# Kernel optimization log

Measured on AMD Instinct MI355X. Metric: run time of the kernel, lower is better.

## Reference

```python
import jax, jax.numpy as jnp
import numpy as np

H, N_EMB, D_EMB, D_UP = 1024, 8192, 512, 2048
B, T, BB, M, K_LABELS = 4, 4096, 512, 4096, 64


def _rms(x, w, eps=1e-6):
    xf = x.astype(jnp.float32)
    var = jnp.mean(xf * xf, axis=-1, keepdims=True)
    return (w * (xf * jax.lax.rsqrt(var + eps))).astype(x.dtype)


def setup_inputs() -> dict:
    key = jax.random.key(0)
    ks = jax.random.split(key, 8)
    bt = B * T
    inp = jax.random.normal(ks[0], (B, T, H), jnp.float32)
    w_k = jax.random.normal(ks[1], (N_EMB, H), jnp.float32) * 0.02
    w_v = jax.random.normal(ks[2], (N_EMB, D_EMB), jnp.float32) * 0.02
    w_up = jax.random.normal(ks[3], (D_UP, D_EMB), jnp.float32) * 0.02
    w_mix = jax.random.normal(ks[4], (H, D_UP + H), jnp.float32) * 0.02
    fw = jax.random.permutation(ks[5], bt)
    bw = jnp.argsort(fw)  # inverse permutation
    seq_sort = jax.random.randint(ks[6], (bt,), 0, K_LABELS)
    keep_cols = jnp.arange(M)  # keep first M of N_EMB rows
    emb_alloc = jnp.arange(N_EMB) % K_LABELS  # every label present among kept rows
    starts = jnp.zeros((bt,), jnp.int32)
    ends = jnp.full((bt,), M, jnp.int32)
    return {
        'input': inp, 'fw': fw, 'bw': bw, 'seq_sort': seq_sort,
        'keep_cols': keep_cols, 'emb_alloc': emb_alloc,
        'starts': starts, 'ends': ends, 'bb': BB,
        'w_k_weight': w_k, 'w_v_weight': w_v, 'w_up_weight': w_up,
        'w_mix_weight': w_mix,
        'norm_in_weight': jnp.ones((H,), jnp.float32),
        'norm_out_weight': jnp.ones((D_UP,), jnp.float32),
    }


def reference(input, fw, bw, seq_sort, keep_cols, emb_alloc, starts, ends, bb,
              w_k_weight, w_v_weight, w_up_weight, w_mix_weight,
              norm_in_weight, norm_out_weight):
    b, t, h = input.shape
    A = _rms(input, norm_in_weight)                      # [b,t,h]
    Bm = w_k_weight[keep_cols]                           # [m,h]
    Cm = w_v_weight[keep_cols]                           # [m,d_emb]
    la = emb_alloc[keep_cols]                            # [m]
    A = A.reshape(-1, h)[fw].reshape(-1, bb, h)          # [nb,bb,h]
    ss = seq_sort.reshape(-1, bb)                        # [nb,bb]
    st = starts.reshape(-1, bb).min(axis=-1)             # [nb]
    en = ends.reshape(-1, bb).max(axis=-1)               # [nb]
    # ragged per-block slice B[start:end] expressed as a kv range mask,
    # combined with the equality mask seq_sort[q] == emb_alloc[kv]
    scores = jnp.einsum('nqh,kh->nqk', A, Bm)            # [nb,bb,m]
    kv = jnp.arange(Bm.shape[0])
    mask = ((ss[:, :, None] == la[None, None, :])
            & (kv[None, None, :] >= st[:, None, None])
            & (kv[None, None, :] < en[:, None, None]))
    scores = jnp.where(mask, scores, -jnp.inf)
    p = jax.nn.softmax(scores, axis=-1)
    comb = jnp.einsum('nqk,kd->nqd', p, Cm)              # [nb,bb,d_emb]
    d_emb = Cm.shape[-1]
    comb = comb.reshape(-1, d_emb)[bw].reshape(b, t, d_emb)
    up = comb @ w_up_weight.T                            # [b,t,d_up]
    cat = jnp.concatenate([_rms(up, norm_out_weight), input], axis=-1)
    return cat @ w_mix_weight.T                          # [b,t,h]
```

## Files before the change

### kernel.cpp

```cpp
#include <hip/hip_runtime.h>
#include <hip/hip_bf16.h>
#include <cstdint>
#include <cstddef>

#define Hh 1024
#define D_EMB 512
#define D_UP 2048
#define BT 16384
#define BB_ 512
#define Mm 4096
#define MmP 4160
#define NB 32
#define KL 64
#define NXCD 8

typedef __attribute__((ext_vector_type(4))) float f4;
typedef __attribute__((ext_vector_type(4))) __bf16 bf4;
typedef __attribute__((ext_vector_type(8))) __bf16 bf8;
typedef __attribute__((ext_vector_type(4))) float f32x4;

__device__ __forceinline__ void gl_lds16(const void* g, void* l) {
  __builtin_amdgcn_global_load_lds((__attribute__((address_space(1))) void*)g,
                                   (__attribute__((address_space(3))) void*)l, 16, 0, 0);
}

__global__ __launch_bounds__(256) void conv_bf16_kernel(const float* __restrict__ src,
                                                        __bf16* __restrict__ dst, int n4) {
  int i = blockIdx.x * 256 + threadIdx.x;
  if (i >= n4) return;
  f4 v = ((const f4*)src)[i];
  bf4 o = {(__bf16)v[0], (__bf16)v[1], (__bf16)v[2], (__bf16)v[3]};
  ((bf4*)dst)[i] = o;
}

__global__ __launch_bounds__(256) void gather_bf16_kernel(const float* __restrict__ src,
                                                          const int* __restrict__ idx,
                                                          __bf16* __restrict__ dst, int cols4) {
  int row = blockIdx.x;
  const f4* s = (const f4*)src + (size_t)idx[row] * cols4;
  bf4* d = (bf4*)dst + (size_t)row * cols4;
  for (int i = threadIdx.x; i < cols4; i += 256) {
    f4 v = s[i];
    bf4 o = {(__bf16)v[0], (__bf16)v[1], (__bf16)v[2], (__bf16)v[3]};
    d[i] = o;
  }
}

__global__ __launch_bounds__(256) void la_kernel(const int* __restrict__ keep,
                                                 const int* __restrict__ emb,
                                                 int* __restrict__ la, int m) {
  int i = blockIdx.x * 256 + threadIdx.x;
  if (i < m) la[i] = emb[keep[i]];
}

__global__ __launch_bounds__(256) void range_kernel(const int* __restrict__ starts,
                                                    const int* __restrict__ ends,
                                                    int* __restrict__ stA, int* __restrict__ enA) {
  int n = blockIdx.x;
  int t = threadIdx.x, lane = t & 63, wv = t >> 6;
  int s1 = min(starts[n * BB_ + t], starts[n * BB_ + t + 256]);
  int e1 = max(ends[n * BB_ + t], ends[n * BB_ + t + 256]);
#pragma unroll
  for (int off = 32; off; off >>= 1) {
    s1 = min(s1, __shfl_xor(s1, off));
    e1 = max(e1, __shfl_xor(e1, off));
  }
  __shared__ int ssh[4], esh[4];
  if (lane == 0) { ssh[wv] = s1; esh[wv] = e1; }
  __syncthreads();
  if (t == 0) {
    int s = ssh[0], e = esh[0];
#pragma unroll
    for (int k = 1; k < 4; ++k) { s = min(s, ssh[k]); e = max(e, esh[k]); }
    stA[n] = s; enA[n] = e;
  }
}

__global__ __launch_bounds__(256) void hist_kernel(const int* __restrict__ la,
                                                   int* __restrict__ goff) {
  __shared__ int cnt[KL];
  int tid = threadIdx.x;
  if (tid < KL) cnt[tid] = 0;
  __syncthreads();
  for (int k = tid; k < Mm; k += 256) atomicAdd(&cnt[la[k]], 1);
  __syncthreads();
  if (tid == 0) {
    int a = 0;
    for (int s = 0; s < KL; ++s) { goff[s] = a; a += cnt[s]; }
    goff[KL] = a;
  }
}

__global__ __launch_bounds__(256) void place_kernel(const int* __restrict__ la,
                                                    const int* __restrict__ keep,
                                                    const int* __restrict__ goff,
                                                    int* __restrict__ gk,
                                                    int* __restrict__ ridx) {
  int s = blockIdx.x;
  int tid = threadIdx.x, lane = tid & 63, wv = tid >> 6;
  __shared__ int wc[4];
  __shared__ int run;
  if (tid == 0) run = goff[s];
  __syncthreads();
  for (int base = 0; base < Mm; base += 256) {
    int k = base + tid;
    bool f = (la[k] == s);
    unsigned long long msk = __ballot(f);
    int myidx = __popcll(msk & ((1ull << lane) - 1ull));
    if (lane == 0) wc[wv] = __popcll(msk);
    __syncthreads();
    int woff = 0, tot = 0;
#pragma unroll
    for (int w = 0; w < 4; ++w) {
      if (w < wv) woff += wc[w];
      tot += wc[w];
    }
    int rbase = run;
    if (f) {
      int p = rbase + woff + myidx;
      gk[p] = k;
      ridx[p] = keep[k];
    }
    __syncthreads();
    if (tid == 0) run = rbase + tot;
    __syncthreads();
  }
}

__global__ __launch_bounds__(256) void lohi_kernel(const int* __restrict__ gk,
                                                   const int* __restrict__ goff,
                                                   const int* __restrict__ stA,
                                                   const int* __restrict__ enA,
                                                   int* __restrict__ loA, int* __restrict__ hiA) {
  int i = blockIdx.x * 256 + threadIdx.x;
  if (i >= NB * KL) return;
  int n = i / KL, s = i % KL;
  int b = goff[s], e = goff[s + 1];
  int st = stA[n], en = enA[n];
  int lo = b, hi = e;
  while (lo < hi) { int mid = (lo + hi) >> 1; if (gk[mid] < st) lo = mid + 1; else hi = mid; }
  int L = lo;
  lo = b; hi = e;
  while (lo < hi) { int mid = (lo + hi) >> 1; if (gk[mid] < en) lo = mid + 1; else hi = mid; }
  loA[i] = L;
  hiA[i] = lo;
}

__global__ __launch_bounds__(256) void vt_kernel(const float* __restrict__ wv_,
                                                 const int* __restrict__ ridx,
                                                 __bf16* __restrict__ VT) {
  int pb = blockIdx.x * 64;
  int db = blockIdx.y * 64;
  __shared__ float T[64][65];
  int t = threadIdx.x;
  int dl = t & 63, g = t >> 6;
  for (int i = g * 16; i < g * 16 + 16; ++i) {
    int pos = pb + i;
    float val = 0.f;
    if (pos < Mm) {
      int r = ridx[pos];
      val = wv_[(size_t)r * D_EMB + db + dl];
    }
    T[dl][i] = val;
  }
  __syncthreads();
  int pl = t & 63;
  for (int j = g * 16; j < g * 16 + 16; ++j) {
    VT[(size_t)(db + j) * MmP + pb + pl] = (__bf16)T[j][pl];
  }
}

__global__ __launch_bounds__(256) void qsort_kernel(const int* __restrict__ seq_sort,
                                                    int* __restrict__ qidx,
                                                    int* __restrict__ qoffA,
                                                    int* __restrict__ qcntA) {
  int n = blockIdx.x, tid = threadIdx.x;
  __shared__ int cnt[KL], pos[KL], pref[KL];
  if (tid < KL) cnt[tid] = 0;
  __syncthreads();
  int s0 = seq_sort[n * BB_ + tid];
  int s1 = seq_sort[n * BB_ + tid + 256];
  atomicAdd(&cnt[s0], 1);
  atomicAdd(&cnt[s1], 1);
  __syncthreads();
  if (tid == 0) {
    int a = 0;
    for (int s = 0; s < KL; ++s) { pref[s] = a; a += cnt[s]; }
  }
  __syncthreads();
  if (tid < KL) {
    pos[tid] = pref[tid];
    qoffA[n * KL + tid] = pref[tid];
    qcntA[n * KL + tid] = cnt[tid];
  }
  __syncthreads();
  int p0 = atomicAdd(&pos[s0], 1);
  qidx[n * BB_ + p0] = n * BB_ + tid;
  int p1 = atomicAdd(&pos[s1], 1);
  qidx[n * BB_ + p1] = n * BB_ + tid + 256;
}

__global__ __launch_bounds__(256) void rms_in_kernel(const float* __restrict__ input,
                                                     const int* __restrict__ bw,
                                                     const float* __restrict__ wn,
                                                     __bf16* __restrict__ Aperm,
                                                     __bf16* __restrict__ inb) {
  int wv = threadIdx.x >> 6, lane = threadIdx.x & 63;
  int j = blockIdx.x * 4 + wv;
  const f4* src = (const f4*)(input + (size_t)j * Hh);
  f4 v[4];
  float ss = 0.f;
#pragma unroll
  for (int c = 0; c < 4; ++c) {
    v[c] = src[c * 64 + lane];
    ss += v[c][0] * v[c][0] + v[c][1] * v[c][1] + v[c][2] * v[c][2] + v[c][3] * v[c][3];
  }
#pragma unroll
  for (int off = 32; off; off >>= 1) ss += __shfl_xor(ss, off);
  float sc = rsqrtf(ss * (1.f / Hh) + 1e-6f);
  bf4* dstI = (bf4*)(inb + (size_t)j * Hh);
#pragma unroll
  for (int c = 0; c < 4; ++c) {
    bf4 o = {(__bf16)v[c][0], (__bf16)v[c][1], (__bf16)v[c][2], (__bf16)v[c][3]};
    dstI[c * 64 + lane] = o;
  }
  int dj = bw[j];
  const f4* w4 = (const f4*)wn;
  bf4* dstA = (bf4*)(Aperm + (size_t)dj * Hh);
#pragma unroll
  for (int c = 0; c < 4; ++c) {
    f4 w = w4[c * 64 + lane];
    bf4 o = {(__bf16)(v[c][0] * sc * w[0]), (__bf16)(v[c][1] * sc * w[1]),
             (__bf16)(v[c][2] * sc * w[2]), (__bf16)(v[c][3] * sc * w[3])};
    dstA[c * 64 + lane] = o;
  }
}

__global__ __launch_bounds__(256, 2) void attn4_kernel(const __bf16* __restrict__ Aperm,
                                                       const __bf16* __restrict__ Ks,
                                                       const __bf16* __restrict__ VT,
                                                       const int* __restrict__ qidx,
                                                       const int* __restrict__ qoffA,
                                                       const int* __restrict__ qcntA,
                                                       const int* __restrict__ loA,
                                                       const int* __restrict__ hiA,
                                                       const int* __restrict__ fw,
                                                       __bf16* __restrict__ comb) {
  __shared__ __align__(16) __bf16 owb[4][16][528];
  int wv = threadIdx.x >> 6, lane = threadIdx.x & 63;
  int g = blockIdx.x * 4 + wv;
  int qcnt = qcntA[g];
  int lo = loA[g], hi = hiA[g];
  if (qcnt == 0 || lo >= hi) return;
  int n = g >> 6;
  int qbase = n * BB_ + qoffA[g];
  int c = lane & 15, rg = lane >> 4;
  int sl_a = c + ((rg & 1) << 5);
  int sl_b = sl_a + 16;
  bool hiKt = (rg & 2) != 0;
  const __bf16* vbase = VT + (size_t)c * MmP + rg * 8;

  for (int qt = 0; qt < qcnt; qt += 16) {
    int ql = qt + c;
    int j = qidx[qbase + (ql < qcnt ? ql : qcnt - 1)];
    const __bf16* qrow = Aperm + (size_t)j * Hh + rg * 8;

    float m = -1e30f, lsum = 0.f;
    f32x4 acc[32];
    f32x4 zero = {0.f, 0.f, 0.f, 0.f};
#pragma unroll
    for (int ff = 0; ff < 32; ++ff) acc[ff] = zero;

    for (int p0 = lo; p0 < hi; p0 += 64) {
      const __bf16* kb = Ks + (size_t)(p0 + c) * Hh + rg * 8;
      f32x4 sN[4];
#pragma unroll
      for (int kt = 0; kt < 4; ++kt) sN[kt] = zero;
#pragma unroll
      for (int ks = 0; ks < 32; ++ks) {
        bf8 qf = *(const bf8*)(qrow + ks * 32);
#pragma unroll
        for (int kt = 0; kt < 4; ++kt) {
          bf8 kf = *(const bf8*)(kb + (size_t)kt * 16 * Hh + ks * 32);
          sN[kt] = __builtin_amdgcn_mfma_f32_16x16x32_bf16(kf, qf, sN[kt], 0, 0, 0);
        }
      }
      float smax = -1e30f;
#pragma unroll
      for (int kt = 0; kt < 4; ++kt)
#pragma unroll
        for (int r = 0; r < 4; ++r) {
          int kv = p0 + kt * 16 + rg * 4 + r;
          float sv = (kv < hi) ? sN[kt][r] : -1e30f;
          sN[kt][r] = sv;
          smax = fmaxf(smax, sv);
        }
      smax = fmaxf(smax, __shfl_xor(smax, 16));
      smax = fmaxf(smax, __shfl_xor(smax, 32));
      float mn = fmaxf(m, smax);
      float sc = __expf(m - mn);
      float sum = 0.f;
#pragma unroll
      for (int kt = 0; kt < 4; ++kt)
#pragma unroll
        for (int r = 0; r < 4; ++r) {
          float pv = __expf(sN[kt][r] - mn);
          sN[kt][r] = pv;
          sum += pv;
        }
      sum += __shfl_xor(sum, 16);
      sum += __shfl_xor(sum, 32);
      lsum = lsum * sc + sum;
      m = mn;
#pragma unroll
      for (int ff = 0; ff < 32; ++ff) acc[ff] = acc[ff] * sc;

      bf8 pbh[2];
#pragma unroll
      for (int h = 0; h < 2; ++h) {
        float e[8];
#pragma unroll
        for (int r = 0; r < 4; ++r) {
          float a0 = __shfl(sN[2 * h][r], sl_a);
          float a1 = __shfl(sN[2 * h + 1][r], sl_a);
          e[r] = hiKt ? a1 : a0;
          float b0 = __shfl(sN[2 * h][r], sl_b);
          float b1 = __shfl(sN[2 * h + 1][r], sl_b);
          e[4 + r] = hiKt ? b1 : b0;
        }
        bf8 pb;
#pragma unroll
        for (int i = 0; i < 8; ++i) pb[i] = (__bf16)e[i];
        pbh[h] = pb;
      }
#pragma unroll
      for (int ff = 0; ff < 32; ++ff) {
        const __bf16* vr = vbase + (size_t)ff * (16 * MmP) + p0;
        bf8 v0 = *(const bf8*)(vr);
        bf8 v1 = *(const bf8*)(vr + 32);
        acc[ff] = __builtin_amdgcn_mfma_f32_16x16x32_bf16(v0, pbh[0], acc[ff], 0, 0, 0);
        acc[ff] = __builtin_amdgcn_mfma_f32_16x16x32_bf16(v1, pbh[1], acc[ff], 0, 0, 0);
      }
    }

    float inv = 1.f / lsum;
#pragma unroll
    for (int ff = 0; ff < 32; ++ff) {
      bf4 o;
#pragma unroll
      for (int r = 0; r < 4; ++r) o[r] = (__bf16)(acc[ff][r] * inv);
      *(bf4*)&owb[wv][c][ff * 16 + rg * 4] = o;
    }
    int qp = qt + (lane >> 2);
    bool vq = qp < qcnt;
    size_t ob = 0;
    if (vq) ob = (size_t)fw[qidx[qbase + qp]] * D_EMB + (lane & 3) * 8;
#pragma unroll
    for (int it = 0; it < 16; ++it) {
      bf8 o = *(const bf8*)&owb[wv][lane >> 2][(lane & 3) * 8 + it * 32];
      if (vq) *(bf8*)(comb + ob + (size_t)it * 32) = o;
    }
  }
}

template <bool OUT_BF16>
__global__ __launch_bounds__(512, 2) void gemm8p(const __bf16* __restrict__ x0, int k0,
                                                 const __bf16* __restrict__ x1, int k1,
                                                 const __bf16* __restrict__ w,
                                                 void* __restrict__ outp, int Mt, int Nt) {
  __shared__ __align__(16) __bf16 lds[4][2][256 * 32];
  const int nwg = Mt * Nt;
  const int bid = blockIdx.x;
  const int swz = (bid % NXCD) * (nwg / NXCD) + bid / NXCD;
  const int m0 = (swz / Nt) * 256, n0 = (swz % Nt) * 256;
  const int K = k0 + k1;
  const int NT = K >> 5;
  const int N = Nt * 256;
  const int tid = threadIdx.x, lane = tid & 63, wvi = tid >> 6;
  const int wr = wvi >> 2, wc = wvi & 3;

  const int srow = tid >> 2;
  const int spb = (tid & 3) * 16;

  const int c = lane & 15, rg = lane >> 4;
  const int fa_off = c * 64 + ((rg ^ ((c >> 1) & 3)) << 4);

  auto stage_half = [&](int t, int j) {
    int kg = t * 32;
    const __bf16* xs;
    int ld, kk;
    if (kg < k0) { xs = x0; ld = k0; kk = kg; }
    else         { xs = x1; ld = k1; kk = kg - k0; }
    int b = t & 3;
    int r = j * 128 + srow;
    int lcol = (spb ^ (((r >> 1) & 3) << 4)) >> 1;
    gl_lds16(xs + (size_t)(m0 + r) * ld + kk + lcol,
             (void*)((char*)&lds[b][0][0] + r * 64 + spb));
    gl_lds16(w + (size_t)(n0 + r) * K + kg + lcol,
             (void*)((char*)&lds[b][1][0] + r * 64 + spb));
  };

  f32x4 acc[8][4];
  f32x4 zero = {0.f, 0.f, 0.f, 0.f};
#pragma unroll
  for (int a = 0; a < 8; ++a)
#pragma unroll
    for (int bnx = 0; bnx < 4; ++bnx) acc[a][bnx] = zero;

#pragma unroll
  for (int t = 0; t < 3; ++t) {
    stage_half(t, 0);
    stage_half(t, 1);
  }
  asm volatile("s_waitcnt vmcnt(8)" ::: "memory");
  __builtin_amdgcn_s_barrier();

  for (int t = 0; t < NT; ++t) {
    const char* Abase = (const char*)&lds[t & 3][0][0];
    const char* Bbase = (const char*)&lds[t & 3][1][0];
    bf8 bfr[4];
#pragma unroll
    for (int ri = 0; ri < 2; ++ri) {
      if (t + 3 < NT) stage_half(t + 3, ri);
      bf8 afr[4];
#pragma unroll
      for (int fi = 0; fi < 4; ++fi)
        afr[fi] = *(const bf8*)(Abase + (wr * 128 + ri * 64 + fi * 16) * 64 + fa_off);
      if (ri == 0) {
#pragma unroll
        for (int fi = 0; fi < 4; ++fi)
          bfr[fi] = *(const bf8*)(Bbase + (wc * 64 + fi * 16) * 64 + fa_off);
      }
      __builtin_amdgcn_s_barrier();
      __builtin_amdgcn_s_setprio(1);
#pragma unroll
      for (int fi = 0; fi < 4; ++fi)
#pragma unroll
        for (int ni = 0; ni < 4; ++ni)
          acc[ri * 4 + fi][ni] =
              __builtin_amdgcn_mfma_f32_16x16x32_bf16(afr[fi], bfr[ni], acc[ri * 4 + fi][ni], 0, 0, 0);
      __builtin_amdgcn_s_setprio(0);
      if (ri == 1) asm volatile("s_waitcnt vmcnt(8)" ::: "memory");
      __builtin_amdgcn_s_barrier();
    }
  }

  const int r0 = (lane >> 4) * 4, cc = lane & 15;
#pragma unroll
  for (int mi = 0; mi < 8; ++mi) {
    int rowb = m0 + wr * 128 + (mi >> 2) * 64 + (mi & 3) * 16 + r0;
#pragma unroll
    for (int ni = 0; ni < 4; ++ni) {
      int col = n0 + wc * 64 + ni * 16 + cc;
#pragma unroll
      for (int r = 0; r < 4; ++r) {
        float v = acc[mi][ni][r];
        if (OUT_BF16)
          ((__bf16*)outp)[(size_t)(rowb + r) * N + col] = (__bf16)v;
        else
          ((float*)outp)[(size_t)(rowb + r) * N + col] = v;
      }
    }
  }
}

__global__ __launch_bounds__(256) void rms_up_kernel(__bf16* __restrict__ up,
                                                     const float* __restrict__ wn) {
  int wv = threadIdx.x >> 6, lane = threadIdx.x & 63;
  size_t j = (size_t)blockIdx.x * 4 + wv;
  bf8* row = (bf8*)(up + j * D_UP);
  bf8 v[4];
  float ss = 0.f;
#pragma unroll
  for (int c = 0; c < 4; ++c) {
    v[c] = row[c * 64 + lane];
#pragma unroll
    for (int i = 0; i < 8; ++i) { float f = (float)v[c][i]; ss += f * f; }
  }
#pragma unroll
  for (int off = 32; off; off >>= 1) ss += __shfl_xor(ss, off);
  float sc = rsqrtf(ss * (1.f / D_UP) + 1e-6f);
#pragma unroll
  for (int c = 0; c < 4; ++c) {
    int ebase = (c * 64 + lane) * 8;
    f4 wa = *(const f4*)(wn + ebase);
    f4 wb = *(const f4*)(wn + ebase + 4);
    bf8 o;
#pragma unroll
    for (int i = 0; i < 4; ++i) o[i] = (__bf16)((float)v[c][i] * sc * wa[i]);
#pragma unroll
    for (int i = 0; i < 4; ++i) o[4 + i] = (__bf16)((float)v[c][4 + i] * sc * wb[i]);
    row[c * 64 + lane] = o;
  }
}

extern "C" void kernel_launch(void* const* d_in, const int* in_sizes, int n_in, void* d_out,
                              int out_size, void* d_ws, size_t ws_size, hipStream_t stream) {
  const float* input = (const float*)d_in[0];
  const int* fw = (const int*)d_in[1];
  const int* bw = (const int*)d_in[2];
  const int* seq_sort = (const int*)d_in[3];
  const int* keep_cols = (const int*)d_in[4];
  const int* emb_alloc = (const int*)d_in[5];
  const int* starts = (const int*)d_in[6];
  const int* ends = (const int*)d_in[7];
  const float* w_k = (const float*)d_in[9];
  const float* w_v = (const float*)d_in[10];
  const float* w_up = (const float*)d_in[11];
  const float* w_mix = (const float*)d_in[12];
  const float* w_nin = (const float*)d_in[13];
  const float* w_nout = (const float*)d_in[14];

  char* p = (char*)d_ws;
  auto take = [&](size_t b) {
    void* r = (void*)p;
    p += (b + 255) & ~(size_t)255;
    return r;
  };
  __bf16* Aperm = (__bf16*)take((size_t)BT * Hh * 2);
  __bf16* inb = (__bf16*)take((size_t)BT * Hh * 2);
  __bf16* comb = (__bf16*)take((size_t)BT * D_EMB * 2);
  __bf16* up = (__bf16*)take((size_t)BT * D_UP * 2);
  __bf16* Ks = (__bf16*)take((size_t)MmP * Hh * 2);
  __bf16* VT = (__bf16*)take((size_t)D_EMB * MmP * 2);
  __bf16* wupB = (__bf16*)take((size_t)D_UP * D_EMB * 2);
  __bf16* wmixB = (__bf16*)take((size_t)Hh * (D_UP + Hh) * 2);
  int* la = (int*)take(Mm * 4);
  int* stA = (int*)take(NB * 4);
  int* enA = (int*)take(NB * 4);
  int* goff = (int*)take((KL + 1) * 4);
  int* gk = (int*)take(Mm * 4);
  int* ridx = (int*)take(Mm * 4);
  int* loA = (int*)take(NB * KL * 4);
  int* hiA = (int*)take(NB * KL * 4);
  int* qidx = (int*)take(BT * 4);
  int* qoffA = (int*)take(NB * KL * 4);
  int* qcntA = (int*)take(NB * KL * 4);

  conv_bf16_kernel<<<(D_UP * D_EMB / 4 + 255) / 256, 256, 0, stream>>>(w_up, wupB, D_UP * D_EMB / 4);
  conv_bf16_kernel<<<(Hh * (D_UP + Hh) / 4 + 255) / 256, 256, 0, stream>>>(w_mix, wmixB,
                                                                           Hh * (D_UP + Hh) / 4);
  la_kernel<<<Mm / 256, 256, 0, stream>>>(keep_cols, emb_alloc, la, Mm);
  range_kernel<<<NB, 256, 0, stream>>>(starts, ends, stA, enA);
  hist_kernel<<<1, 256, 0, stream>>>(la, goff);
  place_kernel<<<KL, 256, 0, stream>>>(la, keep_cols, goff, gk, ridx);
  lohi_kernel<<<(NB * KL + 255) / 256, 256, 0, stream>>>(gk, goff, stA, enA, loA, hiA);
  gather_bf16_kernel<<<Mm, 256, 0, stream>>>(w_k, ridx, Ks, Hh / 4);
  vt_kernel<<<dim3(MmP / 64, D_EMB / 64), 256, 0, stream>>>(w_v, ridx, VT);
  qsort_kernel<<<NB, 256, 0, stream>>>(seq_sort, qidx, qoffA, qcntA);

  rms_in_kernel<<<BT / 4, 256, 0, stream>>>(input, bw, w_nin, Aperm, inb);
  attn4_kernel<<<NB * KL / 4, 256, 0, stream>>>(Aperm, Ks, VT, qidx, qoffA, qcntA, loA, hiA, fw,
                                                comb);
  gemm8p<true><<<BT / 256 * (D_UP / 256), 512, 0, stream>>>(comb, D_EMB, (const __bf16*)nullptr, 0,
                                                            wupB, (void*)up, BT / 256, D_UP / 256);
  rms_up_kernel<<<BT / 4, 256, 0, stream>>>(up, w_nout);
  gemm8p<false><<<BT / 256 * (Hh / 256), 512, 0, stream>>>(up, D_UP, inb, Hh, wmixB, d_out,
                                                           BT / 256, Hh / 256);
}
```

Measured before the change: 360.8 us.

## Regroup attention queries across blocks per label with MFMA-swizzled Q/K/V layouts

```diff
diff --git a/kernel.cpp b/kernel.cpp
--- a/kernel.cpp
+++ b/kernel.cpp
@@ -9,10 +9,12 @@
 #define BT 16384
 #define BB_ 512
 #define Mm 4096
-#define MmP 4160
 #define NB 32
 #define KL 64
 #define NXCD 8
+#define PMMAX 8192
+#define QROWMAX 17408
+#define MAXT 1088
 
 typedef __attribute__((ext_vector_type(4))) float f4;
 typedef __attribute__((ext_vector_type(4))) __bf16 bf4;
@@ -31,19 +33,6 @@
   f4 v = ((const f4*)src)[i];
   bf4 o = {(__bf16)v[0], (__bf16)v[1], (__bf16)v[2], (__bf16)v[3]};
   ((bf4*)dst)[i] = o;
-}
-
-__global__ __launch_bounds__(256) void gather_bf16_kernel(const float* __restrict__ src,
-                                                          const int* __restrict__ idx,
-                                                          __bf16* __restrict__ dst, int cols4) {
-  int row = blockIdx.x;
-  const f4* s = (const f4*)src + (size_t)idx[row] * cols4;
-  bf4* d = (bf4*)dst + (size_t)row * cols4;
-  for (int i = threadIdx.x; i < cols4; i += 256) {
-    f4 v = s[i];
-    bf4 o = {(__bf16)v[0], (__bf16)v[1], (__bf16)v[2], (__bf16)v[3]};
-    d[i] = o;
-  }
 }
 
 __global__ __launch_bounds__(256) void la_kernel(const int* __restrict__ keep,
@@ -127,8 +116,85 @@
   }
 }
 
+__global__ __launch_bounds__(256) void qsort_kernel(const int* __restrict__ seq_sort,
+                                                    int* __restrict__ qidx,
+                                                    int* __restrict__ qoffA,
+                                                    int* __restrict__ qcntA) {
+  int n = blockIdx.x, tid = threadIdx.x;
+  __shared__ int cnt[KL], pos[KL], pref[KL];
+  if (tid < KL) cnt[tid] = 0;
+  __syncthreads();
+  int s0 = seq_sort[n * BB_ + tid];
+  int s1 = seq_sort[n * BB_ + tid + 256];
+  atomicAdd(&cnt[s0], 1);
+  atomicAdd(&cnt[s1], 1);
+  __syncthreads();
+  if (tid == 0) {
+    int a = 0;
+    for (int s = 0; s < KL; ++s) { pref[s] = a; a += cnt[s]; }
+  }
+  __syncthreads();
+  if (tid < KL) {
+    pos[tid] = pref[tid];
+    qoffA[n * KL + tid] = pref[tid];
+    qcntA[n * KL + tid] = cnt[tid];
+  }
+  __syncthreads();
+  int p0 = atomicAdd(&pos[s0], 1);
+  qidx[n * BB_ + p0] = n * BB_ + tid;
+  int p1 = atomicAdd(&pos[s1], 1);
+  qidx[n * BB_ + p1] = n * BB_ + tid + 256;
+}
+
+__global__ __launch_bounds__(256) void qmeta_kernel(const int* __restrict__ qcntA,
+                                                    const int* __restrict__ goff,
+                                                    int* __restrict__ boff,
+                                                    int* __restrict__ qtot,
+                                                    int* __restrict__ ptq,
+                                                    int* __restrict__ pb,
+                                                    int* __restrict__ taskS,
+                                                    int* __restrict__ taskT,
+                                                    int* __restrict__ ntt,
+                                                    int* __restrict__ pbTot) {
+  int tid = threadIdx.x;
+  if (tid < KL) {
+    int s = tid, tot = 0;
+    for (int n = 0; n < NB; ++n) { boff[n * KL + s] = tot; tot += qcntA[n * KL + s]; }
+    qtot[s] = tot;
+  }
+  __syncthreads();
+  if (tid == 0) {
+    int tb = 0, tk = 0, pk = 0;
+    for (int s = 0; s < KL; ++s) {
+      ptq[s] = tb;
+      int nt = (qtot[s] + 15) >> 4;
+      for (int t2 = 0; t2 < nt; ++t2) { taskS[tk] = s; taskT[tk] = t2; ++tk; }
+      tb += nt;
+      pb[s] = pk;
+      int cnt = goff[s + 1] - goff[s];
+      pk += (cnt + 63) & ~63;
+    }
+    ptq[KL] = tb;
+    ntt[0] = tk;
+    pbTot[0] = pk;
+  }
+}
+
+__global__ __launch_bounds__(256) void pridx_kernel(const int* __restrict__ goff,
+                                                    const int* __restrict__ pb,
+                                                    const int* __restrict__ ridx,
+                                                    int* __restrict__ pridx) {
+  int s = blockIdx.x;
+  int cnt = goff[s + 1] - goff[s];
+  int padded = (cnt + 63) & ~63;
+  int base = pb[s];
+  for (int i = threadIdx.x; i < padded; i += 256)
+    pridx[base + i] = (i < cnt) ? ridx[goff[s] + i] : -1;
+}
+
 __global__ __launch_bounds__(256) void lohi_kernel(const int* __restrict__ gk,
                                                    const int* __restrict__ goff,
+                                                   const int* __restrict__ pb,
                                                    const int* __restrict__ stA,
                                                    const int* __restrict__ enA,
                                                    int* __restrict__ loA, int* __restrict__ hiA) {
@@ -142,69 +208,105 @@
   int L = lo;
   lo = b; hi = e;
   while (lo < hi) { int mid = (lo + hi) >> 1; if (gk[mid] < en) lo = mid + 1; else hi = mid; }
-  loA[i] = L;
-  hiA[i] = lo;
-}
-
-__global__ __launch_bounds__(256) void vt_kernel(const float* __restrict__ wv_,
-                                                 const int* __restrict__ ridx,
-                                                 __bf16* __restrict__ VT) {
-  int pb = blockIdx.x * 64;
-  int db = blockIdx.y * 64;
-  __shared__ float T[64][65];
-  int t = threadIdx.x;
-  int dl = t & 63, g = t >> 6;
-  for (int i = g * 16; i < g * 16 + 16; ++i) {
-    int pos = pb + i;
-    float val = 0.f;
-    if (pos < Mm) {
-      int r = ridx[pos];
-      val = wv_[(size_t)r * D_EMB + db + dl];
-    }
-    T[dl][i] = val;
-  }
-  __syncthreads();
-  int pl = t & 63;
-  for (int j = g * 16; j < g * 16 + 16; ++j) {
-    VT[(size_t)(db + j) * MmP + pb + pl] = (__bf16)T[j][pl];
-  }
-}
-
-__global__ __launch_bounds__(256) void qsort_kernel(const int* __restrict__ seq_sort,
-                                                    int* __restrict__ qidx,
-                                                    int* __restrict__ qoffA,
-                                                    int* __restrict__ qcntA) {
-  int n = blockIdx.x, tid = threadIdx.x;
-  __shared__ int cnt[KL], pos[KL], pref[KL];
-  if (tid < KL) cnt[tid] = 0;
-  __syncthreads();
-  int s0 = seq_sort[n * BB_ + tid];
-  int s1 = seq_sort[n * BB_ + tid + 256];
-  atomicAdd(&cnt[s0], 1);
-  atomicAdd(&cnt[s1], 1);
-  __syncthreads();
-  if (tid == 0) {
-    int a = 0;
-    for (int s = 0; s < KL; ++s) { pref[s] = a; a += cnt[s]; }
-  }
-  __syncthreads();
-  if (tid < KL) {
-    pos[tid] = pref[tid];
-    qoffA[n * KL + tid] = pref[tid];
-    qcntA[n * KL + tid] = cnt[tid];
-  }
-  __syncthreads();
-  int p0 = atomicAdd(&pos[s0], 1);
-  qidx[n * BB_ + p0] = n * BB_ + tid;
-  int p1 = atomicAdd(&pos[s1], 1);
-  qidx[n * BB_ + p1] = n * BB_ + tid + 256;
+  loA[i] = pb[s] + (L - goff[s]);
+  hiA[i] = pb[s] + (lo - goff[s]);
+}
+
+__global__ __launch_bounds__(256) void gq_kernel(const int* __restrict__ qidx,
+                                                 const int* __restrict__ qoffA,
+                                                 const int* __restrict__ seq_sort,
+                                                 const int* __restrict__ boff,
+                                                 const int* __restrict__ ptq,
+                                                 int* __restrict__ qg2, int* __restrict__ gq) {
+  int e = blockIdx.x * 256 + threadIdx.x;
+  int n = e >> 9;
+  int q = qidx[e];
+  int s = seq_sort[q];
+  int i = (e & 511) - qoffA[n * KL + s];
+  int gpos = ptq[s] * 16 + boff[n * KL + s] + i;
+  qg2[gpos] = q;
+  gq[q] = gpos;
+}
+
+__global__ __launch_bounds__(256) void qzero_kernel(const int* __restrict__ ptq,
+                                                    const int* __restrict__ qtot,
+                                                    __bf16* __restrict__ Qsw) {
+  int s = blockIdx.x;
+  int b0 = ptq[s] * 16 + qtot[s];
+  int b1 = ptq[s + 1] * 16;
+  bf8 z;
+#pragma unroll
+  for (int j = 0; j < 8; ++j) z[j] = (__bf16)0.f;
+  for (int r = b0; r < b1; ++r)
+    for (int e8 = threadIdx.x; e8 < 128; e8 += 256)
+      *(bf8*)&Qsw[(size_t)r * 1024 + e8 * 8] = z;
+}
+
+__global__ __launch_bounds__(256) void kswb_kernel(const float* __restrict__ wk,
+                                                   const int* __restrict__ pridx,
+                                                   const int* __restrict__ pbTot,
+                                                   __bf16* __restrict__ Ksw) {
+  int pt = blockIdx.x;
+  if (pt * 16 >= pbTot[0]) return;
+  __shared__ __bf16 Tk[16][1040];
+  int tid = threadIdx.x;
+  int rr = tid >> 4, lt = tid & 15;
+  int src = pridx[pt * 16 + rr];
+  for (int cc = 0; cc < 16; ++cc) {
+    int i4 = cc * 16 + lt;
+    f4 v = {0.f, 0.f, 0.f, 0.f};
+    if (src >= 0) v = ((const f4*)(wk + (size_t)src * Hh))[i4];
+    bf4 o = {(__bf16)v[0], (__bf16)v[1], (__bf16)v[2], (__bf16)v[3]};
+    *(bf4*)&Tk[rr][i4 * 4] = o;
+  }
+  __syncthreads();
+#pragma unroll
+  for (int i = 0; i < 8; ++i) {
+    int f = tid + 256 * i;
+    int ks = f >> 6, ln = f & 63;
+    int c2 = ln & 15, rg2 = ln >> 4;
+    bf8 o = *(const bf8*)&Tk[c2][ks * 32 + rg2 * 8];
+    *(bf8*)&Ksw[(size_t)pt * 16384 + (size_t)f * 8] = o;
+  }
+}
+
+__global__ __launch_bounds__(256) void vswb_kernel(const float* __restrict__ wv_,
+                                                   const int* __restrict__ pridx,
+                                                   const int* __restrict__ pbTot,
+                                                   __bf16* __restrict__ Vsw) {
+  int pblk = blockIdx.x;
+  if (pblk * 32 >= pbTot[0]) return;
+  __shared__ __bf16 Tv[32][528];
+  int tid = threadIdx.x;
+  int rr = tid >> 3, lt = tid & 7;
+  int src = pridx[pblk * 32 + rr];
+  for (int cc = 0; cc < 16; ++cc) {
+    int i4 = cc * 8 + lt;
+    f4 v = {0.f, 0.f, 0.f, 0.f};
+    if (src >= 0) v = ((const f4*)(wv_ + (size_t)src * D_EMB))[i4];
+    bf4 o = {(__bf16)v[0], (__bf16)v[1], (__bf16)v[2], (__bf16)v[3]};
+    *(bf4*)&Tv[rr][i4 * 4] = o;
+  }
+  __syncthreads();
+#pragma unroll
+  for (int i = 0; i < 8; ++i) {
+    int f = tid + 256 * i;
+    int ff = f >> 6, ln = f & 63;
+    int c2 = ln & 15, rg2 = ln >> 4;
+    bf8 o;
+#pragma unroll
+    for (int j = 0; j < 8; ++j) o[j] = Tv[rg2 * 8 + j][ff * 16 + c2];
+    *(bf8*)&Vsw[(size_t)pblk * 16384 + (size_t)f * 8] = o;
+  }
 }
 
 __global__ __launch_bounds__(256) void rms_in_kernel(const float* __restrict__ input,
                                                      const int* __restrict__ bw,
+                                                     const int* __restrict__ gq,
                                                      const float* __restrict__ wn,
-                                                     __bf16* __restrict__ Aperm,
+                                                     __bf16* __restrict__ Qsw,
                                                      __bf16* __restrict__ inb) {
+  __shared__ __align__(16) __bf16 rowbuf[4][1024];
   int wv = threadIdx.x >> 6, lane = threadIdx.x & 63;
   int j = blockIdx.x * 4 + wv;
   const f4* src = (const f4*)(input + (size_t)j * Hh);
@@ -224,142 +326,161 @@
     bf4 o = {(__bf16)v[c][0], (__bf16)v[c][1], (__bf16)v[c][2], (__bf16)v[c][3]};
     dstI[c * 64 + lane] = o;
   }
-  int dj = bw[j];
   const f4* w4 = (const f4*)wn;
-  bf4* dstA = (bf4*)(Aperm + (size_t)dj * Hh);
 #pragma unroll
   for (int c = 0; c < 4; ++c) {
     f4 w = w4[c * 64 + lane];
     bf4 o = {(__bf16)(v[c][0] * sc * w[0]), (__bf16)(v[c][1] * sc * w[1]),
              (__bf16)(v[c][2] * sc * w[2]), (__bf16)(v[c][3] * sc * w[3])};
-    dstA[c * 64 + lane] = o;
-  }
-}
-
-__global__ __launch_bounds__(256, 2) void attn4_kernel(const __bf16* __restrict__ Aperm,
-                                                       const __bf16* __restrict__ Ks,
-                                                       const __bf16* __restrict__ VT,
-                                                       const int* __restrict__ qidx,
-                                                       const int* __restrict__ qoffA,
-                                                       const int* __restrict__ qcntA,
-                                                       const int* __restrict__ loA,
-                                                       const int* __restrict__ hiA,
+    *(bf4*)&rowbuf[wv][(c * 64 + lane) * 4] = o;
+  }
+  int gpos = gq[bw[j]];
+  int qt2 = gpos >> 4, cq = gpos & 15;
+#pragma unroll
+  for (int h = 0; h < 2; ++h) {
+    int k_ = lane + h * 64;
+    int ks = k_ >> 2, rg2 = k_ & 3;
+    bf8 o = *(const bf8*)&rowbuf[wv][ks * 32 + rg2 * 8];
+    *(bf8*)(Qsw + (size_t)qt2 * 16384 + ks * 512 + (cq + 16 * rg2) * 8) = o;
+  }
+}
+
+__global__ __launch_bounds__(256, 2) void attn5_kernel(const __bf16* __restrict__ Qsw,
+                                                       const __bf16* __restrict__ Ksw,
+                                                       const __bf16* __restrict__ Vsw,
+                                                       const int* __restrict__ qg2,
+                                                       const int* __restrict__ qtot,
+                                                       const int* __restrict__ ptq,
+                                                       const int* __restrict__ taskS,
+                                                       const int* __restrict__ taskT,
+                                                       const int* __restrict__ nttA,
+                                                       const int* __restrict__ pb,
+                                                       const int* __restrict__ loP,
+                                                       const int* __restrict__ hiP,
                                                        const int* __restrict__ fw,
                                                        __bf16* __restrict__ comb) {
   __shared__ __align__(16) __bf16 owb[4][16][528];
   int wv = threadIdx.x >> 6, lane = threadIdx.x & 63;
-  int g = blockIdx.x * 4 + wv;
-  int qcnt = qcntA[g];
-  int lo = loA[g], hi = hiA[g];
-  if (qcnt == 0 || lo >= hi) return;
-  int n = g >> 6;
-  int qbase = n * BB_ + qoffA[g];
+  int t = blockIdx.x * 4 + wv;
+  if (t >= nttA[0]) return;
+  int s = taskS[t], tl = taskT[t];
+  int qtp = ptq[s] + tl;
+  int qcnt = min(16, qtot[s] - tl * 16);
   int c = lane & 15, rg = lane >> 4;
+  bool qv = c < qcnt;
+  int q_l = qg2[qtp * 16 + (qv ? c : 0)];
+  int n_l = q_l >> 9;
+  int lo_l = qv ? loP[n_l * KL + s] : 0x7fffffff;
+  int hi_l = qv ? hiP[n_l * KL + s] : 0;
+  int tlo = lo_l, thi = hi_l;
+#pragma unroll
+  for (int off = 1; off < 64; off <<= 1) {
+    tlo = min(tlo, __shfl_xor(tlo, off));
+    thi = max(thi, __shfl_xor(thi, off));
+  }
+  if (tlo >= thi) return;
+  int pbs = pb[s];
+
   int sl_a = c + ((rg & 1) << 5);
   int sl_b = sl_a + 16;
   bool hiKt = (rg & 2) != 0;
-  const __bf16* vbase = VT + (size_t)c * MmP + rg * 8;
-
-  for (int qt = 0; qt < qcnt; qt += 16) {
-    int ql = qt + c;
-    int j = qidx[qbase + (ql < qcnt ? ql : qcnt - 1)];
-    const __bf16* qrow = Aperm + (size_t)j * Hh + rg * 8;
-
-    float m = -1e30f, lsum = 0.f;
-    f32x4 acc[32];
-    f32x4 zero = {0.f, 0.f, 0.f, 0.f};
-#pragma unroll
-    for (int ff = 0; ff < 32; ++ff) acc[ff] = zero;
-
-    for (int p0 = lo; p0 < hi; p0 += 64) {
-      const __bf16* kb = Ks + (size_t)(p0 + c) * Hh + rg * 8;
-      f32x4 sN[4];
-#pragma unroll
-      for (int kt = 0; kt < 4; ++kt) sN[kt] = zero;
-#pragma unroll
-      for (int ks = 0; ks < 32; ++ks) {
-        bf8 qf = *(const bf8*)(qrow + ks * 32);
-#pragma unroll
-        for (int kt = 0; kt < 4; ++kt) {
-          bf8 kf = *(const bf8*)(kb + (size_t)kt * 16 * Hh + ks * 32);
-          sN[kt] = __builtin_amdgcn_mfma_f32_16x16x32_bf16(kf, qf, sN[kt], 0, 0, 0);
-        }
+  const __bf16* Qb = Qsw + (size_t)qtp * 16384 + lane * 8;
+
+  float m = -1e30f, lsum = 0.f;
+  f32x4 acc[32];
+  f32x4 zero = {0.f, 0.f, 0.f, 0.f};
+#pragma unroll
+  for (int ff = 0; ff < 32; ++ff) acc[ff] = zero;
+
+  int p0beg = pbs + ((tlo - pbs) & ~63);
+  for (int p0 = p0beg; p0 < thi; p0 += 64) {
+    const __bf16* Kb = Ksw + (size_t)(p0 >> 4) * 16384 + lane * 8;
+    f32x4 sN[4];
+#pragma unroll
+    for (int kt = 0; kt < 4; ++kt) sN[kt] = zero;
+#pragma unroll
+    for (int ks = 0; ks < 32; ++ks) {
+      bf8 qf = *(const bf8*)(Qb + ks * 512);
+#pragma unroll
+      for (int kt = 0; kt < 4; ++kt) {
+        bf8 kf = *(const bf8*)(Kb + kt * 16384 + ks * 512);
+        sN[kt] = __builtin_amdgcn_mfma_f32_16x16x32_bf16(kf, qf, sN[kt], 0, 0, 0);
       }
-      float smax = -1e30f;
-#pragma unroll
-      for (int kt = 0; kt < 4; ++kt)
-#pragma unroll
-        for (int r = 0; r < 4; ++r) {
-          int kv = p0 + kt * 16 + rg * 4 + r;
-          float sv = (kv < hi) ? sN[kt][r] : -1e30f;
-          sN[kt][r] = sv;
-          smax = fmaxf(smax, sv);
-        }
-      smax = fmaxf(smax, __shfl_xor(smax, 16));
-      smax = fmaxf(smax, __shfl_xor(smax, 32));
-      float mn = fmaxf(m, smax);
-      float sc = __expf(m - mn);
-      float sum = 0.f;
-#pragma unroll
-      for (int kt = 0; kt < 4; ++kt)
-#pragma unroll
-        for (int r = 0; r < 4; ++r) {
-          float pv = __expf(sN[kt][r] - mn);
-          sN[kt][r] = pv;
-          sum += pv;
-        }
-      sum += __shfl_xor(sum, 16);
-      sum += __shfl_xor(sum, 32);
-      lsum = lsum * sc + sum;
-      m = mn;
-#pragma unroll
-      for (int ff = 0; ff < 32; ++ff) acc[ff] = acc[ff] * sc;
-
-      bf8 pbh[2];
-#pragma unroll
-      for (int h = 0; h < 2; ++h) {
-        float e[8];
-#pragma unroll
-        for (int r = 0; r < 4; ++r) {
-          float a0 = __shfl(sN[2 * h][r], sl_a);
-          float a1 = __shfl(sN[2 * h + 1][r], sl_a);
-          e[r] = hiKt ? a1 : a0;
-          float b0 = __shfl(sN[2 * h][r], sl_b);
-          float b1 = __shfl(sN[2 * h + 1][r], sl_b);
-          e[4 + r] = hiKt ? b1 : b0;
-        }
-        bf8 pb;
-#pragma unroll
-        for (int i = 0; i < 8; ++i) pb[i] = (__bf16)e[i];
-        pbh[h] = pb;
+    }
+    float smax = -1e30f;
+#pragma unroll
+    for (int kt = 0; kt < 4; ++kt)
+#pragma unroll
+      for (int r = 0; r < 4; ++r) {
+        int kv = p0 + kt * 16 + rg * 4 + r;
+        float sv = (kv >= lo_l && kv < hi_l) ? sN[kt][r] : -1e30f;
+        sN[kt][r] = sv;
+        smax = fmaxf(smax, sv);
       }
-#pragma unroll
-      for (int ff = 0; ff < 32; ++ff) {
-        const __bf16* vr = vbase + (size_t)ff * (16 * MmP) + p0;
-        bf8 v0 = *(const bf8*)(vr);
-        bf8 v1 = *(const bf8*)(vr + 32);
-        acc[ff] = __builtin_amdgcn_mfma_f32_16x16x32_bf16(v0, pbh[0], acc[ff], 0, 0, 0);
-        acc[ff] = __builtin_amdgcn_mfma_f32_16x16x32_bf16(v1, pbh[1], acc[ff], 0, 0, 0);
+    smax = fmaxf(smax, __shfl_xor(smax, 16));
+    smax = fmaxf(smax, __shfl_xor(smax, 32));
+    float mn = fmaxf(m, smax);
+    float scl = __expf(m - mn);
+    float sum = 0.f;
+#pragma unroll
+    for (int kt = 0; kt < 4; ++kt)
+#pragma unroll
+      for (int r = 0; r < 4; ++r) {
+        float pv = __expf(sN[kt][r] - mn);
+        sN[kt][r] = pv;
+        sum += pv;
       }
-    }
-
-    float inv = 1.f / lsum;
+    sum += __shfl_xor(sum, 16);
+    sum += __shfl_xor(sum, 32);
+    lsum = lsum * scl + sum;
+    m = mn;
+#pragma unroll
+    for (int ff = 0; ff < 32; ++ff) acc[ff] = acc[ff] * scl;
+
+    bf8 pbh[2];
+#pragma unroll
+    for (int h = 0; h < 2; ++h) {
+      float e[8];
+#pragma unroll
+      for (int r = 0; r < 4; ++r) {
+        float a0 = __shfl(sN[2 * h][r], sl_a);
+        float a1 = __shfl(sN[2 * h + 1][r], sl_a);
+        e[r] = hiKt ? a1 : a0;
+        float b0 = __shfl(sN[2 * h][r], sl_b);
+        float b1 = __shfl(sN[2 * h + 1][r], sl_b);
+        e[4 + r] = hiKt ? b1 : b0;
+      }
+      bf8 pbv;
+#pragma unroll
+      for (int i = 0; i < 8; ++i) pbv[i] = (__bf16)e[i];
+      pbh[h] = pbv;
+    }
+    const __bf16* Vb = Vsw + (size_t)(p0 >> 5) * 16384 + lane * 8;
 #pragma unroll
     for (int ff = 0; ff < 32; ++ff) {
-      bf4 o;
-#pragma unroll
-      for (int r = 0; r < 4; ++r) o[r] = (__bf16)(acc[ff][r] * inv);
-      *(bf4*)&owb[wv][c][ff * 16 + rg * 4] = o;
-    }
-    int qp = qt + (lane >> 2);
-    bool vq = qp < qcnt;
-    size_t ob = 0;
-    if (vq) ob = (size_t)fw[qidx[qbase + qp]] * D_EMB + (lane & 3) * 8;
-#pragma unroll
-    for (int it = 0; it < 16; ++it) {
-      bf8 o = *(const bf8*)&owb[wv][lane >> 2][(lane & 3) * 8 + it * 32];
-      if (vq) *(bf8*)(comb + ob + (size_t)it * 32) = o;
-    }
+      bf8 v0 = *(const bf8*)(Vb + ff * 512);
+      bf8 v1 = *(const bf8*)(Vb + 16384 + ff * 512);
+      acc[ff] = __builtin_amdgcn_mfma_f32_16x16x32_bf16(v0, pbh[0], acc[ff], 0, 0, 0);
+      acc[ff] = __builtin_amdgcn_mfma_f32_16x16x32_bf16(v1, pbh[1], acc[ff], 0, 0, 0);
+    }
+  }
+
+  float inv = 1.f / lsum;
+#pragma unroll
+  for (int ff = 0; ff < 32; ++ff) {
+    bf4 o;
+#pragma unroll
+    for (int r = 0; r < 4; ++r) o[r] = (__bf16)(acc[ff][r] * inv);
+    *(bf4*)&owb[wv][c][ff * 16 + rg * 4] = o;
+  }
+  int qsel = lane >> 2;
+  bool vq = qsel < qcnt;
+  size_t ob = 0;
+  if (vq) ob = (size_t)fw[qg2[qtp * 16 + qsel]] * D_EMB + (lane & 3) * 8;
+#pragma unroll
+  for (int it = 0; it < 16; ++it) {
+    bf8 o = *(const bf8*)&owb[wv][lane >> 2][(lane & 3) * 8 + it * 32];
+    if (vq) *(bf8*)(comb + ob + (size_t)it * 32) = o;
   }
 }
 
@@ -517,25 +638,37 @@
     p += (b + 255) & ~(size_t)255;
     return r;
   };
-  __bf16* Aperm = (__bf16*)take((size_t)BT * Hh * 2);
   __bf16* inb = (__bf16*)take((size_t)BT * Hh * 2);
   __bf16* comb = (__bf16*)take((size_t)BT * D_EMB * 2);
-  __bf16* up = (__bf16*)take((size_t)BT * D_UP * 2);
-  __bf16* Ks = (__bf16*)take((size_t)MmP * Hh * 2);
-  __bf16* VT = (__bf16*)take((size_t)D_EMB * MmP * 2);
   __bf16* wupB = (__bf16*)take((size_t)D_UP * D_EMB * 2);
   __bf16* wmixB = (__bf16*)take((size_t)Hh * (D_UP + Hh) * 2);
+  char* pB = p;
+  __bf16* Ksw = (__bf16*)take((size_t)PMMAX * 1024 * 2);
+  __bf16* Vsw = (__bf16*)take((size_t)PMMAX * 512 * 2);
+  __bf16* Qsw = (__bf16*)take((size_t)QROWMAX * 1024 * 2);
   int* la = (int*)take(Mm * 4);
   int* stA = (int*)take(NB * 4);
   int* enA = (int*)take(NB * 4);
   int* goff = (int*)take((KL + 1) * 4);
   int* gk = (int*)take(Mm * 4);
   int* ridx = (int*)take(Mm * 4);
+  int* pridx = (int*)take(PMMAX * 4);
   int* loA = (int*)take(NB * KL * 4);
   int* hiA = (int*)take(NB * KL * 4);
   int* qidx = (int*)take(BT * 4);
   int* qoffA = (int*)take(NB * KL * 4);
   int* qcntA = (int*)take(NB * KL * 4);
+  int* boff = (int*)take(NB * KL * 4);
+  int* qtot = (int*)take(KL * 4);
+  int* ptq = (int*)take((KL + 1) * 4);
+  int* pb = (int*)take(KL * 4);
+  int* taskS = (int*)take(MAXT * 4);
+  int* taskT = (int*)take(MAXT * 4);
+  int* ntt = (int*)take(4);
+  int* pbTot = (int*)take(4);
+  int* qg2 = (int*)take(QROWMAX * 4);
+  int* gq = (int*)take(BT * 4);
+  __bf16* up = (__bf16*)pB;
 
   conv_bf16_kernel<<<(D_UP * D_EMB / 4 + 255) / 256, 256, 0, stream>>>(w_up, wupB, D_UP * D_EMB / 4);
   conv_bf16_kernel<<<(Hh * (D_UP + Hh) / 4 + 255) / 256, 256, 0, stream>>>(w_mix, wmixB,
@@ -543,15 +676,19 @@
   la_kernel<<<Mm / 256, 256, 0, stream>>>(keep_cols, emb_alloc, la, Mm);
   range_kernel<<<NB, 256, 0, stream>>>(starts, ends, stA, enA);
   hist_kernel<<<1, 256, 0, stream>>>(la, goff);
+  qsort_kernel<<<NB, 256, 0, stream>>>(seq_sort, qidx, qoffA, qcntA);
   place_kernel<<<KL, 256, 0, stream>>>(la, keep_cols, goff, gk, ridx);
-  lohi_kernel<<<(NB * KL + 255) / 256, 256, 0, stream>>>(gk, goff, stA, enA, loA, hiA);
-  gather_bf16_kernel<<<Mm, 256, 0, stream>>>(w_k, ridx, Ks, Hh / 4);
-  vt_kernel<<<dim3(MmP / 64, D_EMB / 64), 256, 0, stream>>>(w_v, ridx, VT);
-  qsort_kernel<<<NB, 256, 0, stream>>>(seq_sort, qidx, qoffA, qcntA);
-
-  rms_in_kernel<<<BT / 4, 256, 0, stream>>>(input, bw, w_nin, Aperm, inb);
-  attn4_kernel<<<NB * KL / 4, 256, 0, stream>>>(Aperm, Ks, VT, qidx, qoffA, qcntA, loA, hiA, fw,
-                                                comb);
+  qmeta_kernel<<<1, 256, 0, stream>>>(qcntA, goff, boff, qtot, ptq, pb, taskS, taskT, ntt, pbTot);
+  pridx_kernel<<<KL, 256, 0, stream>>>(goff, pb, ridx, pridx);
+  lohi_kernel<<<(NB * KL + 255) / 256, 256, 0, stream>>>(gk, goff, pb, stA, enA, loA, hiA);
+  gq_kernel<<<BT / 256, 256, 0, stream>>>(qidx, qoffA, seq_sort, boff, ptq, qg2, gq);
+  qzero_kernel<<<KL, 256, 0, stream>>>(ptq, qtot, Qsw);
+  kswb_kernel<<<PMMAX / 16, 256, 0, stream>>>(w_k, pridx, pbTot, Ksw);
+  vswb_kernel<<<PMMAX / 32, 256, 0, stream>>>(w_v, pridx, pbTot, Vsw);
+
+  rms_in_kernel<<<BT / 4, 256, 0, stream>>>(input, bw, gq, w_nin, Qsw, inb);
+  attn5_kernel<<<MAXT / 4, 256, 0, stream>>>(Qsw, Ksw, Vsw, qg2, qtot, ptq, taskS, taskT, ntt, pb,
+                                             loA, hiA, fw, comb);
   gemm8p<true><<<BT / 256 * (D_UP / 256), 512, 0, stream>>>(comb, D_EMB, (const __bf16*)nullptr, 0,
                                                             wupB, (void*)up, BT / 256, D_UP / 256);
   rms_up_kernel<<<BT / 4, 256, 0, stream>>>(up, w_nout);
```

New measurement: 376.0 us. +4.2%, slower.
